# Kernel tuning notes

Measured on AMD Instinct MI355X. Metric: run time of the kernel, lower is better.

The kernel has to match this reference:

```python
import jax, jax.numpy as jnp
import numpy as np

N, SP, SI, K = 256, 64, 32, 8
CIN, C, HEADS, DH = 32, 128, 8, 16
G = 32
OCC_THRESH = 0.7

def _lrelu(x):
    return jax.nn.leaky_relu(x, 0.01)

def _ln(x):
    mu = x.mean(-1, keepdims=True)
    var = ((x - mu) ** 2).mean(-1, keepdims=True)
    return (x - mu) * jax.lax.rsqrt(var + 1e-5)

def _interp3d(vol, coords):
    # vol [C,D,H,W]; coords [...,3] in (z,y,x) voxel-index units -> [..., C]
    v = jnp.moveaxis(vol, 0, -1)
    Dv, Hv, Wv = v.shape[0], v.shape[1], v.shape[2]
    z = jnp.clip(coords[..., 0], 0.0, Dv - 1.0)
    y = jnp.clip(coords[..., 1], 0.0, Hv - 1.0)
    x = jnp.clip(coords[..., 2], 0.0, Wv - 1.0)
    z0 = jnp.floor(z).astype(jnp.int32); y0 = jnp.floor(y).astype(jnp.int32); x0 = jnp.floor(x).astype(jnp.int32)
    z1 = jnp.minimum(z0 + 1, Dv - 1); y1 = jnp.minimum(y0 + 1, Hv - 1); x1 = jnp.minimum(x0 + 1, Wv - 1)
    wz = (z - z0)[..., None]; wy = (y - y0)[..., None]; wx = (x - x0)[..., None]
    c00 = v[z0, y0, x0] * (1 - wx) + v[z0, y0, x1] * wx
    c01 = v[z0, y1, x0] * (1 - wx) + v[z0, y1, x1] * wx
    c10 = v[z1, y0, x0] * (1 - wx) + v[z1, y0, x1] * wx
    c11 = v[z1, y1, x0] * (1 - wx) + v[z1, y1, x1] * wx
    return (c00 * (1 - wy) + c01 * wy) * (1 - wz) + (c10 * (1 - wy) + c11 * wy) * wz

def _tpoints(T, p):
    return p @ T[:3, :3].T + T[:3, 3]

def _rot(T, v):
    return v @ T[:3, :3].T

def _ray_box(o, d, obj_from_cam, dim):
    oo = _tpoints(obj_from_cam, o); dd = _rot(obj_from_cam, d)
    half = dim / 2
    invd = 1.0 / jnp.where(jnp.abs(dd) < 1e-9, 1e-9, dd)
    t0 = (-half - oo) * invd; t1 = (half - oo) * invd
    tlo = jnp.minimum(t0, t1).max(-1); thi = jnp.maximum(t0, t1).min(-1)
    valid = thi >= jnp.maximum(tlo, 0.0)
    return jnp.where(valid, tlo, jnp.inf)

def _attn_block(x, Wqkv, bqkv, Wo, bo, Wf1, bf1, Wf2, bf2):
    # pre-LN MHA over axis -2, then pre-LN FFN; residuals
    h = _ln(x)
    qkv = h @ Wqkv + bqkv
    q, k, v = jnp.split(qkv, 3, axis=-1)
    hd = lambda a: a.reshape(a.shape[:-1] + (HEADS, DH))
    q, k, v = hd(q), hd(k), hd(v)
    s = jnp.einsum('...qhd,...khd->...hqk', q, k) / jnp.sqrt(jnp.float32(DH))
    a = jax.nn.softmax(s, axis=-1)
    o = jnp.einsum('...hqk,...khd->...qhd', a, v)
    o = o.reshape(o.shape[:-2] + (HEADS * DH,)) @ Wo + bo
    x = x + o
    h = _ln(x)
    return x + (_lrelu(h @ Wf1 + bf1) @ Wf2 + bf2)

def setup_inputs() -> dict:
    key = jax.random.key(0)
    ks = jax.random.split(key, 40)
    d = jnp.concatenate([0.25 * (jax.random.uniform(ks[0], (N, 2)) * 2 - 1), jnp.ones((N, 1))], -1)
    rays_d = d / jnp.linalg.norm(d, axis=-1, keepdims=True)
    rays_o = jnp.zeros((N, 3))
    pose = jnp.eye(4).at[2, 3].set(2.0)
    dimension = jnp.ones((3,))
    w = lambda k_, sh: 0.05 * jax.random.normal(k_, sh)
    return {
        'rays_o': rays_o, 'rays_d': rays_d, 'pose': pose, 'dimension': dimension,
        'voxel_probs': jax.random.uniform(ks[1], (G, G, G)),
        'feature_vol': 0.5 * jax.random.normal(ks[2], (CIN, G, G, G)),
        'feature_vol_highres': 0.5 * jax.random.normal(ks[3], (K, 6, G, G, G)),
        'u_primary': jax.random.uniform(ks[4], (N, SP)),
        'u_cat': jax.random.uniform(ks[5], (N, SI)),
        'u_lam': jax.random.uniform(ks[6], (N, SI)),
        'dW1': w(ks[7], (CIN + 1, C)), 'db1': jnp.zeros((C,)),
        'dW2': w(ks[8], (C, 1)), 'db2': jnp.zeros((1,)),
        'rW0': w(ks[9], (CIN + 10, C)), 'rb0': jnp.zeros((C,)),
        'nf_qkv': w(ks[10], (C, 3 * C)), 'nf_qkvb': jnp.zeros((3 * C,)),
        'nf_o': w(ks[11], (C, C)), 'nf_ob': jnp.zeros((C,)),
        'nf_f1': w(ks[12], (C, 2 * C)), 'nf_f1b': jnp.zeros((2 * C,)),
        'nf_f2': w(ks[13], (2 * C, C)), 'nf_f2b': jnp.zeros((C,)),
        'rt_qkv': w(ks[14], (C, 3 * C)), 'rt_qkvb': jnp.zeros((3 * C,)),
        'rt_o': w(ks[15], (C, C)), 'rt_ob': jnp.zeros((C,)),
        'rt_f1': w(ks[16], (C, 2 * C)), 'rt_f1b': jnp.zeros((2 * C,)),
        'rt_f2': w(ks[17], (2 * C, C)), 'rt_f2b': jnp.zeros((C,)),
        'fW': w(ks[18], (C, 3)), 'fb': jnp.zeros((3,)),
        'n_samples_primary': SP, 'n_samples_importance': SI,
    }

def reference(rays_o, rays_d, pose, dimension, voxel_probs, feature_vol, feature_vol_highres,
              u_primary, u_cat, u_lam,
              dW1, db1, dW2, db2, rW0, rb0,
              nf_qkv, nf_qkvb, nf_o, nf_ob, nf_f1, nf_f1b, nf_f2, nf_f2b,
              rt_qkv, rt_qkvb, rt_o, rt_ob, rt_f1, rt_f1b, rt_f2, rt_f2b,
              fW, fb, n_samples_primary, n_samples_importance):
    SPn, SIn = n_samples_primary, n_samples_importance
    ofc = jnp.linalg.inv(pose)  # obj_from_cam
    t_near = _ray_box(rays_o, rays_d, ofc, dimension)
    t_max = t_near + 10.0 * jnp.abs(dimension).sum()
    p_max = rays_o + t_max[:, None] * rays_d
    t_far = t_max - _ray_box(p_max, -rays_d, ofc, dimension)
    m = jnp.isfinite(t_near) & jnp.isfinite(t_far) & (t_far > t_near)
    tn = jnp.where(m, t_near, 0.0); tf = jnp.where(m, t_far, 1.0)
    # stratified primary samples within [t_near, t_far]
    t_coarse = tn[:, None] + (tf - tn)[:, None] * (jnp.arange(SPn, dtype=jnp.float32) + u_primary) / SPn
    get_pts = lambda t: rays_o[:, None] + t[..., None] * rays_d[:, None]
    p_coarse = get_pts(t_coarse)
    def ncoords(p, shp):
        uvz = 0.5 + _tpoints(ofc, p) / dimension
        return uvz[..., ::-1] * (jnp.array(shp, jnp.float32) - 1.0)
    occ_coarse = _interp3d(voxel_probs[None], ncoords(p_coarse, voxel_probs.shape))[..., 0]
    x_coarse = _interp3d(feature_vol, ncoords(p_coarse, feature_vol.shape[-3:]))
    # importance sampling via inverse CDF over adjacent-bin occupancy
    probs = jnp.clip(occ_coarse[:, :-1] + occ_coarse[:, 1:], 1e-12, None)
    cdf = jnp.cumsum(probs, -1)
    cdf = cdf / cdf[:, -1:]
    inds = jnp.clip((u_cat[:, :, None] >= cdf[:, None, :]).sum(-1), 0, SPn - 2)
    t_fine = u_lam * jnp.take_along_axis(t_coarse, inds, -1) + (1 - u_lam) * jnp.take_along_axis(t_coarse, inds + 1, -1)
    p_fine = get_pts(t_fine)
    occ_fine = _interp3d(voxel_probs[None], ncoords(p_fine, voxel_probs.shape))[..., 0]
    x_fine = _interp3d(feature_vol, ncoords(p_fine, feature_vol.shape[-3:]))
    # merge + sort along sample axis
    t_all = jnp.concatenate([t_coarse, t_fine], -1)
    perm = jnp.argsort(t_all, -1)
    t = jnp.take_along_axis(t_all, perm, -1)
    occ = jnp.take_along_axis(jnp.concatenate([occ_coarse, occ_fine], -1), perm, -1)
    p = jnp.take_along_axis(jnp.concatenate([p_coarse, p_fine], -2), perm[..., None], -2)
    x = jnp.take_along_axis(jnp.concatenate([x_coarse, x_fine], -2), perm[..., None], -2)
    # density MLP
    xx = jnp.concatenate([x, occ[..., None]], -1)
    sigma = jax.nn.sigmoid((_lrelu(xx @ dW1 + db1) @ dW2 + db2)[..., 0])
    occ = jnp.where(occ < OCC_THRESH, 0.0, occ)
    alpha = occ * sigma
    # high-res per-view features
    coords_hr = ncoords(p, feature_vol_highres.shape[-3:])
    x_hr = jax.vmap(_interp3d, in_axes=(0, None))(feature_vol_highres, coords_hr)  # [K,N,S,6]
    x_hr = jnp.moveaxis(x_hr, 0, -2)  # [N,S,K,6]
    R = ofc[:3, :3]
    rdo = rays_d @ R.T
    Kv = x_hr.shape[-2]
    bs = x.shape[:2]
    xx2 = jnp.concatenate([
        jnp.broadcast_to(x[:, :, None, :], bs + (Kv, x.shape[-1])),
        x_hr[..., 0:3],
        x_hr[..., 3:6] @ R.T,
        jnp.broadcast_to(rdo[:, None, None, :], bs + (Kv, 3)),
        jnp.broadcast_to(occ[..., None, None], bs + (Kv, 1)),
    ], -1)  # [N,S,K,CIN+10]
    h = xx2 @ rW0 + rb0
    h = _attn_block(h, nf_qkv, nf_qkvb, nf_o, nf_ob, nf_f1, nf_f1b, nf_f2, nf_f2b)  # over views K
    h = h.mean(-2)  # [N,S,C]
    h = _attn_block(h, rt_qkv, rt_qkvb, rt_o, rt_ob, rt_f1, rt_f1b, rt_f2, rt_f2b)  # over samples S
    radiance = jax.nn.sigmoid(h @ fW + fb)  # [N,S,3]
    mk = m[:, None]
    t = jnp.where(mk, t, 0.0)
    occ = jnp.where(mk, occ, 0.0)
    alpha = jnp.where(mk, alpha, 0.0)
    radiance = jnp.where(m[:, None, None], radiance, 0.0)
    # trailing object axis (n_objects=1), matching movedim(0,-1)
    return t[..., None], alpha[..., None], occ[..., None], radiance[..., None]
```

## Files before the change

kernel.cpp:

```cpp
#include <hip/hip_runtime.h>
#include <hip/hip_bf16.h>
#include <cmath>


using bf16 = __hip_bfloat16;
#define DEV __device__ __forceinline__

typedef __attribute__((ext_vector_type(8))) short short8;
typedef __attribute__((ext_vector_type(4))) float f32x4;

DEV float s2f(short s){ unsigned u=((unsigned)(unsigned short)s)<<16; float f; __builtin_memcpy(&f,&u,4); return f; }
DEV short f2s(float f){ bf16 h=__float2bfloat16(f); short r; __builtin_memcpy(&r,&h,2); return r; }

constexpr int NRAY=256, SP=64, SI=32, S=96, KHR=8, CIN=32, C=128, NH=8, DH=16;
constexpr int NT = NRAY*S;
constexpr int MTOT = NT*KHR;

constexpr size_t OFF_RI=0, OFF_TR=9, OFF_M=16, OFF_TN=272, OFF_TF=528, OFF_RDO=784,
  OFF_TS=1552, OFF_OCCS=26128, OFF_OCCT=50704, OFF_CRD=75280, OFF_XS=149008, F32_CNT=935440;

constexpr size_t WT_W0=0, WT_NQKV=8192, WT_NO=57344, WT_NF1=73728, WT_NF2=106496,
  WT_RQKV=139264, WT_RO=188416, WT_RF1=204800, WT_RF2=237568, WT_TOT=270336;
constexpr size_t H2OFF=WT_TOT;
constexpr size_t CHB=H2OFF+(size_t)NT*128;
constexpr size_t RT_TOT=(size_t)NT*512;

struct Corn { int off[8]; float wz, wy, wx; };

DEV void make_corners(float cz, float cy, float cx, Corn& Cn){
  cz=fminf(fmaxf(cz,0.f),31.f); cy=fminf(fmaxf(cy,0.f),31.f); cx=fminf(fmaxf(cx,0.f),31.f);
  int z0=(int)cz, y0=(int)cy, x0=(int)cx;
  int z1=(z0+1<31)?z0+1:31, y1=(y0+1<31)?y0+1:31, x1=(x0+1<31)?x0+1:31;
  Cn.wz=cz-(float)z0; Cn.wy=cy-(float)y0; Cn.wx=cx-(float)x0;
  int zy00=z0*1024+y0*32, zy01=z0*1024+y1*32, zy10=z1*1024+y0*32, zy11=z1*1024+y1*32;
  Cn.off[0]=zy00+x0; Cn.off[1]=zy00+x1;
  Cn.off[2]=zy01+x0; Cn.off[3]=zy01+x1;
  Cn.off[4]=zy10+x0; Cn.off[5]=zy10+x1;
  Cn.off[6]=zy11+x0; Cn.off[7]=zy11+x1;
}

DEV float interp1(const float* __restrict__ vol, const Corn& Cn){
  float v000=vol[Cn.off[0]], v001=vol[Cn.off[1]];
  float v010=vol[Cn.off[2]], v011=vol[Cn.off[3]];
  float v100=vol[Cn.off[4]], v101=vol[Cn.off[5]];
  float v110=vol[Cn.off[6]], v111=vol[Cn.off[7]];
  float wx=Cn.wx, wy=Cn.wy, wz=Cn.wz;
  float c00=v000*(1.f-wx)+v001*wx, c01=v010*(1.f-wx)+v011*wx;
  float c10=v100*(1.f-wx)+v101*wx, c11=v110*(1.f-wx)+v111*wx;
  return (c00*(1.f-wy)+c01*wy)*(1.f-wz) + (c10*(1.f-wy)+c11*wy)*wz;
}

DEV float ray_box(const float* Ri, const float* tr, const float* o3, const float* d3, const float* half){
  float tlo=-INFINITY, thi=INFINITY;
  for(int j=0;j<3;j++){
    float oo=Ri[j*3+0]*o3[0]+Ri[j*3+1]*o3[1]+Ri[j*3+2]*o3[2]+tr[j];
    float dd=Ri[j*3+0]*d3[0]+Ri[j*3+1]*d3[1]+Ri[j*3+2]*d3[2];
    if (fabsf(dd)<1e-9f) dd=1e-9f;
    float inv=1.f/dd;
    float t0=(-half[j]-oo)*inv, t1=(half[j]-oo)*inv;
    tlo=fmaxf(tlo,fminf(t0,t1)); thi=fminf(thi,fmaxf(t0,t1));
  }
  bool valid = thi >= fmaxf(tlo,0.f);
  return valid ? tlo : INFINITY;
}

__global__ __launch_bounds__(64) void k0_setup(
  const float* __restrict__ rays_o, const float* __restrict__ rays_d,
  const float* __restrict__ pose, const float* __restrict__ dimv,
  float* __restrict__ wsf)
{
  __shared__ float Ri[9], tr[3];
  int tid=threadIdx.x; int ray=blockIdx.x*64+tid;
  if(tid==0){
    float P[16];
    for(int j=0;j<16;j++) P[j]=pose[j];
    float a00=P[0],a01=P[1],a02=P[2],a10=P[4],a11=P[5],a12=P[6],a20=P[8],a21=P[9],a22=P[10];
    float c00=a11*a22-a12*a21, c01=a12*a20-a10*a22, c02=a10*a21-a11*a20;
    float det=a00*c00+a01*c01+a02*c02;
    float id=1.f/det;
    Ri[0]=c00*id; Ri[1]=(a02*a21-a01*a22)*id; Ri[2]=(a01*a12-a02*a11)*id;
    Ri[3]=c01*id; Ri[4]=(a00*a22-a02*a20)*id; Ri[5]=(a02*a10-a00*a12)*id;
    Ri[6]=c02*id; Ri[7]=(a01*a20-a00*a21)*id; Ri[8]=(a00*a11-a01*a10)*id;
    float t0=P[3],t1=P[7],t2=P[11];
    tr[0]=-(Ri[0]*t0+Ri[1]*t1+Ri[2]*t2);
    tr[1]=-(Ri[3]*t0+Ri[4]*t1+Ri[5]*t2);
    tr[2]=-(Ri[6]*t0+Ri[7]*t1+Ri[8]*t2);
    if(blockIdx.x==0){
      for(int j=0;j<9;j++) wsf[OFF_RI+j]=Ri[j];
      for(int j=0;j<3;j++) wsf[OFF_TR+j]=tr[j];
    }
  }
  __syncthreads();
  float o3[3],d3[3],dim[3],half[3];
  for(int j=0;j<3;j++){ o3[j]=rays_o[ray*3+j]; d3[j]=rays_d[ray*3+j];
                        dim[j]=dimv[j]; half[j]=0.5f*dim[j]; }
  float tnear=ray_box(Ri,tr,o3,d3,half);
  float tmax=tnear+10.f*(fabsf(dim[0])+fabsf(dim[1])+fabsf(dim[2]));
  float pm[3]={o3[0]+tmax*d3[0], o3[1]+tmax*d3[1], o3[2]+tmax*d3[2]};
  float nd[3]={-d3[0],-d3[1],-d3[2]};
  float tfar=tmax-ray_box(Ri,tr,pm,nd,half);
  bool mm = isfinite(tnear)&&isfinite(tfar)&&(tfar>tnear);
  wsf[OFF_M+ray]=mm?1.f:0.f;
  wsf[OFF_TN+ray]=mm?tnear:0.f;
  wsf[OFF_TF+ray]=mm?tfar:1.f;
  for(int j=0;j<3;j++)
    wsf[OFF_RDO+(size_t)ray*3+j]=Ri[j*3+0]*d3[0]+Ri[j*3+1]*d3[1]+Ri[j*3+2]*d3[2];
}

__global__ __launch_bounds__(128) void k1_sample(
  const float* __restrict__ rays_o, const float* __restrict__ rays_d, const float* __restrict__ dimv,
  const float* __restrict__ voxel, const float* __restrict__ fvol,
  const float* __restrict__ u_p, const float* __restrict__ u_cat, const float* __restrict__ u_lam,
  float* __restrict__ wsf)
{
  int i=blockIdx.x, tid=threadIdx.x;
  __shared__ float Ri[9], tr[3], dim[3], o3[3], d3[3];
  __shared__ float t_all[S], occ_all[S], crd_sh[S][3];
  __shared__ int   coff[S][8];
  __shared__ float cww[S][3];
  __shared__ float cdf[SP];
  __shared__ float totv;
  __shared__ int   rnk[S];
  if(tid<9) Ri[tid]=wsf[OFF_RI+tid];
  if(tid<3){ tr[tid]=wsf[OFF_TR+tid]; dim[tid]=dimv[tid];
             o3[tid]=rays_o[i*3+tid]; d3[tid]=rays_d[i*3+tid]; }
  __syncthreads();
  float tn=wsf[OFF_TN+i], tf=wsf[OFF_TF+i];

  auto do_sample=[&](int s, float t){
    float px=o3[0]+t*d3[0], py=o3[1]+t*d3[1], pz=o3[2]+t*d3[2];
    float q0=Ri[0]*px+Ri[1]*py+Ri[2]*pz+tr[0];
    float q1=Ri[3]*px+Ri[4]*py+Ri[5]*pz+tr[1];
    float q2=Ri[6]*px+Ri[7]*py+Ri[8]*pz+tr[2];
    float cz=(0.5f+q2/dim[2])*31.f;
    float cy=(0.5f+q1/dim[1])*31.f;
    float cx=(0.5f+q0/dim[0])*31.f;
    crd_sh[s][0]=cz; crd_sh[s][1]=cy; crd_sh[s][2]=cx;
    Corn Cn; make_corners(cz,cy,cx,Cn);
    for(int q=0;q<8;q++) coff[s][q]=Cn.off[q];
    cww[s][0]=Cn.wz; cww[s][1]=Cn.wy; cww[s][2]=Cn.wx;
    occ_all[s]=interp1(voxel,Cn);
    t_all[s]=t;
  };

  if(tid<SP){
    float u=u_p[i*SP+tid];
    float t=tn+(tf-tn)*((float)tid+u)*(1.f/64.f);
    do_sample(tid,t);
  }
  __syncthreads();
  if(tid==0){
    float c=0;
    for(int j=0;j<SP-1;j++){ float pr=occ_all[j]+occ_all[j+1]; pr=fmaxf(pr,1e-12f); c+=pr; cdf[j]=c; }
    totv=c;
  }
  __syncthreads();
  if(tid<SP-1) cdf[tid]=cdf[tid]/totv;
  __syncthreads();
  if(tid<SI){
    float u=u_cat[i*SI+tid];
    int cnt=0;
    for(int j=0;j<SP-1;j++) cnt += (u>=cdf[j])?1:0;
    int ind=(cnt<SP-2)?cnt:(SP-2);
    float lam=u_lam[i*SI+tid];
    float tfine=lam*t_all[ind]+(1.f-lam)*t_all[ind+1];
    do_sample(SP+tid,tfine);
  }
  __syncthreads();
  if(tid<S){
    float ts=t_all[tid]; int r=0;
    for(int j=0;j<S;j++){ float tj=t_all[j]; r += (tj<ts || (tj==ts && j<tid)) ? 1:0; }
    rnk[tid]=r;
    size_t base=(size_t)i*S+r;
    wsf[OFF_TS+base]=ts;
    wsf[OFF_OCCS+base]=occ_all[tid];
    wsf[OFF_CRD+base*3+0]=crd_sh[tid][0];
    wsf[OFF_CRD+base*3+1]=crd_sh[tid][1];
    wsf[OFF_CRD+base*3+2]=crd_sh[tid][2];
  }
  __syncthreads();
  for(int idx=tid; idx<S*CIN; idx+=128){
    int s=idx>>5, c=idx&31;
    float wz=cww[s][0], wy=cww[s][1], wx=cww[s][2];
    const float* vc=fvol+(size_t)c*32768;
    float v000=vc[coff[s][0]], v001=vc[coff[s][1]];
    float v010=vc[coff[s][2]], v011=vc[coff[s][3]];
    float v100=vc[coff[s][4]], v101=vc[coff[s][5]];
    float v110=vc[coff[s][6]], v111=vc[coff[s][7]];
    float c00=v000*(1.f-wx)+v001*wx, c01=v010*(1.f-wx)+v011*wx;
    float c10=v100*(1.f-wx)+v101*wx, c11=v110*(1.f-wx)+v111*wx;
    float val=(c00*(1.f-wy)+c01*wy)*(1.f-wz)+(c10*(1.f-wy)+c11*wy)*wz;
    wsf[OFF_XS+((size_t)i*S+rnk[s])*CIN+c]=val;
  }
}

__global__ __launch_bounds__(128) void k2_sigma(
  const float* __restrict__ dW1, const float* __restrict__ db1,
  const float* __restrict__ dW2, const float* __restrict__ db2,
  float* __restrict__ wsf, float* __restrict__ out)
{
  int t=blockIdx.x, tid=threadIdx.x, i=t/S;
  __shared__ float xx[33];
  __shared__ float part[2];
  if(tid<32) xx[tid]=wsf[OFF_XS+(size_t)t*32+tid];
  if(tid==32) xx[32]=wsf[OFF_OCCS+t];
  __syncthreads();
  float acc=db1[tid];
  for(int k=0;k<33;k++) acc=fmaf(xx[k], dW1[k*C+tid], acc);
  acc = acc>=0.f?acc:0.01f*acc;
  float g = acc*dW2[tid];
  for(int off=32;off;off>>=1) g+=__shfl_down(g,off,64);
  if((tid&63)==0) part[tid>>6]=g;
  __syncthreads();
  if(tid==0){
    float z=part[0]+part[1]+db2[0];
    float sg=1.f/(1.f+expf(-z));
    float occ=xx[32];
    float occt=occ<0.7f?0.f:occ;
    float alpha=occt*sg;
    float m=wsf[OFF_M+i];
    float ts=wsf[OFF_TS+t];
    out[t]      =m!=0.f?ts:0.f;
    out[NT+t]   =m!=0.f?alpha:0.f;
    out[2*NT+t] =m!=0.f?occt:0.f;
    wsf[OFF_OCCT+t]=occt;
  }
}

__global__ __launch_bounds__(256) void k_wprep(
  const float* __restrict__ w0, const float* __restrict__ nqkv, const float* __restrict__ no_,
  const float* __restrict__ nf1, const float* __restrict__ nf2,
  const float* __restrict__ rqkv, const float* __restrict__ ro_,
  const float* __restrict__ rf1, const float* __restrict__ rf2,
  short* __restrict__ WT)
{
  int gid = blockIdx.x*256+threadIdx.x;
  if(gid>=(int)WT_TOT) return;
  const float* src; int K,N,Kp; int base;
  if(gid<8192){src=w0;K=42;N=128;Kp=64;base=0;}
  else if(gid<57344){src=nqkv;K=128;N=384;Kp=128;base=8192;}
  else if(gid<73728){src=no_;K=128;N=128;Kp=128;base=57344;}
  else if(gid<106496){src=nf1;K=128;N=256;Kp=128;base=73728;}
  else if(gid<139264){src=nf2;K=256;N=128;Kp=256;base=106496;}
  else if(gid<188416){src=rqkv;K=128;N=384;Kp=128;base=139264;}
  else if(gid<204800){src=ro_;K=128;N=128;Kp=128;base=188416;}
  else if(gid<237568){src=rf1;K=128;N=256;Kp=128;base=204800;}
  else {src=rf2;K=256;N=128;Kp=256;base=237568;}
  int local=gid-base; int n=local/Kp, k=local%Kp;
  WT[gid] = (k<K)? f2s(src[(size_t)k*N+n]) : (short)0;
}

__global__ __launch_bounds__(64) void k_build(
  const float* __restrict__ fvhr, const float* __restrict__ wsf,
  short* __restrict__ X2, int tok0)
{
  int tloc=blockIdx.x, tid=threadIdx.x;
  int t=tok0+tloc, i=t/S;
  __shared__ float hr[KHR][6];
  __shared__ float xf[32];
  __shared__ float RiS[9];
  __shared__ float geo[4];
  __shared__ float crd[3];
  if(tid<9) RiS[tid]=wsf[OFF_RI+tid];
  if(tid>=16&&tid<19) crd[tid-16]=wsf[OFF_CRD+(size_t)t*3+(tid-16)];
  if(tid>=32) xf[tid-32]=wsf[OFF_XS+(size_t)t*32+(tid-32)];
  if(tid==9) geo[0]=wsf[OFF_OCCT+t];
  if(tid>=12&&tid<15) geo[1+(tid-12)]=wsf[OFF_RDO+(size_t)i*3+(tid-12)];
  __syncthreads();
  if(tid<48){
    int k=tid/6, ch=tid%6;
    Corn Cn; make_corners(crd[0],crd[1],crd[2],Cn);
    hr[k][ch]=interp1(fvhr+(size_t)(k*6+ch)*32768, Cn);
  }
  __syncthreads();
  for(int idx=tid; idx<512; idx+=64){
    int k=idx>>6, j=idx&63; float v;
    if(j<32) v=xf[j];
    else if(j<35) v=hr[k][j-32];
    else if(j<38){int r=j-35; v=hr[k][3]*RiS[r*3+0]+hr[k][4]*RiS[r*3+1]+hr[k][5]*RiS[r*3+2];}
    else if(j<41) v=geo[1+(j-38)];
    else if(j==41) v=geo[0];
    else v=0.f;
    X2[(size_t)(tloc*8+k)*64 + j]=f2s(v);
  }
}

template<int K, bool LNA, bool ACT, bool RESID, bool MEAN=false>
__global__ __launch_bounds__(256) void gemm_ln(
  const short* __restrict__ A, const short* __restrict__ Bt,
  const float* __restrict__ bias, const short* __restrict__ Rres,
  short* __restrict__ Cg, int N)
{
  static_assert(!LNA || K==128, "LNA requires K==128");
  constexpr int KSA = (K<128)?K:128;
  constexpr int NSA = K/KSA;
  constexpr int LDA = KSA+8;
  constexpr int LDB = 64+8;
  __shared__ short Al[128*LDA];
  __shared__ short Bl[128*LDB];
  const int tid=threadIdx.x;
  const int bm=blockIdx.x*128, bn=blockIdx.y*128;
  const int lane=tid&63, wave=tid>>6;
  const int wm=(wave>>1)*64, wn=(wave&1)*64;
  const int quad=lane>>4, m16=lane&15;
  f32x4 acc[4][4];
  for(int a=0;a<4;a++) for(int b=0;b<4;b++) acc[a][b]=(f32x4){0.f,0.f,0.f,0.f};

  for(int sa=0; sa<NSA; ++sa){
    if(sa>0) __syncthreads();
    constexpr int CH8=KSA/8;
    for(int it=0; it<(128*CH8)/256; ++it){
      int li=it*256+tid; int row=li/CH8, kc=li%CH8;
      short8 v = *(const short8*)(A + (size_t)(bm+row)*K + sa*KSA + kc*8);
      if constexpr(LNA){
        float f[8]; float ls=0.f,lq=0.f;
        for(int e=0;e<8;e++){ f[e]=s2f(v[e]); ls+=f[e]; lq+=f[e]*f[e]; }
        for(int off=8;off;off>>=1){ ls+=__shfl_xor(ls,off,16); lq+=__shfl_xor(lq,off,16); }
        float mu=ls*(1.f/128.f);
        float var=lq*(1.f/128.f)-mu*mu;
        float rs=rsqrtf(var+1e-5f);
        for(int e=0;e<8;e++) v[e]=f2s((f[e]-mu)*rs);
      }
      *(short8*)&Al[row*LDA+kc*8]=v;
    }
    __syncthreads();
    for(int sb=0; sb<KSA/64; ++sb){
      if(sb>0) __syncthreads();
      for(int it=0; it<4; ++it){
        int li=it*256+tid; int row=li>>3, kc=li&7;
        *(short8*)&Bl[row*LDB+kc*8] =
          *(const short8*)(Bt + (size_t)(bn+row)*K + sa*KSA + sb*64 + kc*8);
      }
      __syncthreads();
      for(int kk=0; kk<64; kk+=32){
        int ka = sb*64+kk;
        short8 af[4], bfv[4];
        for(int im=0; im<4; im++)
          af[im] = *(const short8*)&Al[(wm+im*16+m16)*LDA + ka + quad*8];
        for(int in=0; in<4; in++)
          bfv[in] = *(const short8*)&Bl[(wn+in*16+m16)*LDB + kk + quad*8];
        for(int im=0;im<4;im++)
          for(int in=0;in<4;in++)
            acc[im][in] = __builtin_amdgcn_mfma_f32_16x16x32_bf16(af[im], bfv[in], acc[im][in], 0,0,0);
      }
    }
  }
  for(int in=0;in<4;in++){
    int col = bn + wn + in*16 + m16;
    float bv = bias[col];
    for(int im=0;im<4;im++){
      if constexpr(MEAN){
        float s4=0.f;
        for(int r=0;r<4;r++){
          int grow = bm + wm + im*16 + quad*4 + r;
          float v = acc[im][in][r] + bv;
          if constexpr(RESID) v += s2f(Rres[(size_t)grow*N + col]);
          s4 += v;
        }
        float stok = s4 + __shfl_xor(s4, 16, 64);
        if((quad&1)==0){
          int tok = ((bm + wm + im*16)>>3) + (quad>>1);
          Cg[(size_t)tok*128 + col] = f2s(stok*0.125f);
        }
      } else {
        for(int r=0;r<4;r++){
          int grow = bm + wm + im*16 + quad*4 + r;
          float v = acc[im][in][r] + bv;
          if constexpr(ACT) v = v>=0.f? v : 0.01f*v;
          if constexpr(RESID) v += s2f(Rres[(size_t)grow*N + col]);
          Cg[(size_t)grow*N + col] = f2s(v);
        }
      }
    }
  }
}

__global__ __launch_bounds__(256) void nf_attn(const short* __restrict__ qkv, short* __restrict__ att){
  constexpr int QLD=392;
  __shared__ short Qs[4*8*QLD];
  int t0=blockIdx.x*4, tid=threadIdx.x;
  for(int li=tid; li<1536; li+=256){
    int e=li*8;
    int tok=e/3072, rem=e-tok*3072;
    int j=rem/384, k=rem-j*384;
    *(short8*)&Qs[(tok*8+j)*QLD + k] = *(const short8*)(qkv + (size_t)t0*3072 + e);
  }
  __syncthreads();
  int lt=tid>>6, lane=tid&63;
  int h=lane>>3, q=lane&7;
  const short* base = &Qs[(lt*8)*QLD + h*16];
  float qv[16];
  for(int d=0;d<16;d++) qv[d]=s2f(base[q*QLD+d]);
  float sc[8]; float mx=-INFINITY;
  for(int j=0;j<8;j++){
    float a=0;
    for(int d=0;d<16;d++) a+=qv[d]*s2f(base[j*QLD+128+d]);
    a*=0.25f; sc[j]=a; mx=fmaxf(mx,a);
  }
  float se=0;
  for(int j=0;j<8;j++){ sc[j]=expf(sc[j]-mx); se+=sc[j]; }
  float inv=1.f/se;
  float o[16];
  for(int d=0;d<16;d++) o[d]=0.f;
  for(int j=0;j<8;j++){
    float p=sc[j];
    for(int d=0;d<16;d++) o[d]+=p*s2f(base[j*QLD+256+d]);
  }
  short* ob = att + (size_t)(t0*8 + lt*8 + q)*128 + h*16;
  for(int d=0;d<16;d++) ob[d]=f2s(o[d]*inv);
}

__global__ __launch_bounds__(256) void rt_attn(const short* __restrict__ qkvb, short* __restrict__ attout){
  int b=blockIdx.x; int i=b&255, h0=(b>>8)*4; int tid=threadIdx.x;
  __shared__ float kh[96][64], vh[96][64];
  for(int idx=tid; idx<1536; idx+=256){
    int kv = idx>=768; int l = idx - kv*768;
    int j = l>>3, c = l&7;
    size_t base = ((size_t)(i*96+j))*384 + h0*16 + (kv?256:128) + c*8;
    short8 x = *(const short8*)(qkvb+base);
    float* dst = kv? &vh[j][c*8] : &kh[j][c*8];
    for(int e=0;e<8;e++) dst[e]=s2f(x[e]);
  }
  __syncthreads();
  int jh=tid>>7, t2=tid&127;
  int hh=t2>>5, lq=t2&31, h=h0+hh, r0=lq*3;
  float q[3][16];
  for(int rr=0;rr<3;rr++){
    size_t qb=((size_t)(i*96+r0+rr))*384 + h*16;
    short8 a=*(const short8*)(qkvb+qb), bq=*(const short8*)(qkvb+qb+8);
    for(int e=0;e<8;e++){ q[rr][e]=s2f(a[e]); q[rr][8+e]=s2f(bq[e]); }
  }
  float acc[3][16]; float se[3]={0.f,0.f,0.f};
  for(int rr=0;rr<3;rr++) for(int d=0;d<16;d++) acc[rr][d]=0.f;
  const float* kb=&kh[jh*48][hh*16];
  const float* vb=&vh[jh*48][hh*16];
  for(int j=0;j<48;j++){
    const float* kj = kb + j*64;
    float s0=0.f,s1=0.f,s2=0.f;
    for(int d=0;d<16;d++){ float kv_=kj[d];
      s0=fmaf(q[0][d],kv_,s0); s1=fmaf(q[1][d],kv_,s1); s2=fmaf(q[2][d],kv_,s2); }
    float p0=expf(s0*0.25f), p1=expf(s1*0.25f), p2=expf(s2*0.25f);
    se[0]+=p0; se[1]+=p1; se[2]+=p2;
    const float* vj = vb + j*64;
    for(int d=0;d<16;d++){ float vv=vj[d];
      acc[0][d]=fmaf(p0,vv,acc[0][d]); acc[1][d]=fmaf(p1,vv,acc[1][d]); acc[2][d]=fmaf(p2,vv,acc[2][d]); }
  }
  __syncthreads();
  float* pacc=(float*)kh;
  float* pse =(float*)vh;
  if(jh==1){
    for(int rr=0;rr<3;rr++){
      for(int d=0;d<16;d++) pacc[(t2*3+rr)*16+d]=acc[rr][d];
      pse[t2*3+rr]=se[rr];
    }
  }
  __syncthreads();
  if(jh==0){
    for(int rr=0;rr<3;rr++){
      float sv = se[rr] + pse[t2*3+rr];
      float inv = 1.f/sv;
      short8 o0,o1;
      for(int e=0;e<8;e++){
        float a0=acc[rr][e]   + pacc[(t2*3+rr)*16+e];
        float a1=acc[rr][8+e] + pacc[(t2*3+rr)*16+8+e];
        o0[e]=f2s(a0*inv); o1[e]=f2s(a1*inv);
      }
      size_t ob=((size_t)(i*96+r0+rr))*128 + h*16;
      *(short8*)(attout+ob)=o0;
      *(short8*)(attout+ob+8)=o1;
    }
  }
}

__global__ __launch_bounds__(256) void k_rad(
  const short* __restrict__ h3, const float* __restrict__ fW, const float* __restrict__ fb,
  const float* __restrict__ wsf, float* __restrict__ out)
{
  int t=blockIdx.x*256+threadIdx.x;
  if(t>=NT) return;
  int i=t/S;
  float a0=fb[0], a1=fb[1], a2=fb[2];
  for(int c=0;c<C;c++){
    float hv=s2f(h3[(size_t)t*C+c]);
    a0=fmaf(hv,fW[c*3+0],a0);
    a1=fmaf(hv,fW[c*3+1],a1);
    a2=fmaf(hv,fW[c*3+2],a2);
  }
  float m=wsf[OFF_M+i];
  float r0=1.f/(1.f+expf(-a0)), r1=1.f/(1.f+expf(-a1)), r2=1.f/(1.f+expf(-a2));
  size_t ob=3*(size_t)NT+(size_t)t*3;
  out[ob+0]=m!=0.f?r0:0.f;
  out[ob+1]=m!=0.f?r1:0.f;
  out[ob+2]=m!=0.f?r2:0.f;
}

extern "C" void kernel_launch(void* const* d_in, const int* in_sizes, int n_in,
                              void* d_out, int out_size, void* d_ws, size_t ws_size,
                              hipStream_t stream) {
  (void)in_sizes; (void)n_in; (void)out_size;
  const float* rays_o =(const float*)d_in[0];
  const float* rays_d =(const float*)d_in[1];
  const float* pose   =(const float*)d_in[2];
  const float* dimv   =(const float*)d_in[3];
  const float* voxel  =(const float*)d_in[4];
  const float* fvol   =(const float*)d_in[5];
  const float* fvhr   =(const float*)d_in[6];
  const float* u_p    =(const float*)d_in[7];
  const float* u_cat  =(const float*)d_in[8];
  const float* u_lam  =(const float*)d_in[9];
  const float* dW1    =(const float*)d_in[10];
  const float* db1    =(const float*)d_in[11];
  const float* dW2    =(const float*)d_in[12];
  const float* db2    =(const float*)d_in[13];
  const float* rW0    =(const float*)d_in[14];
  const float* rb0    =(const float*)d_in[15];
  const float* nf_qkv =(const float*)d_in[16];
  const float* nf_qkvb=(const float*)d_in[17];
  const float* nf_o   =(const float*)d_in[18];
  const float* nf_ob  =(const float*)d_in[19];
  const float* nf_f1  =(const float*)d_in[20];
  const float* nf_f1b =(const float*)d_in[21];
  const float* nf_f2  =(const float*)d_in[22];
  const float* nf_f2b =(const float*)d_in[23];
  const float* rt_qkv =(const float*)d_in[24];
  const float* rt_qkvb=(const float*)d_in[25];
  const float* rt_o   =(const float*)d_in[26];
  const float* rt_ob  =(const float*)d_in[27];
  const float* rt_f1  =(const float*)d_in[28];
  const float* rt_f1b =(const float*)d_in[29];
  const float* rt_f2  =(const float*)d_in[30];
  const float* rt_f2b =(const float*)d_in[31];
  const float* fW     =(const float*)d_in[32];
  const float* fb     =(const float*)d_in[33];

  float* wsf=(float*)d_ws;
  short* wsb=(short*)((char*)d_ws + F32_CNT*4);
  float* out=(float*)d_out;

  int nch=8;
  for(int c=1;c<=8;c<<=1){
    size_t mc_=(size_t)MTOT/c;
    size_t region=mc_*640ULL; if(region<RT_TOT) region=RT_TOT;
    size_t need=F32_CNT*4 + 2ULL*(CHB + region);
    if(need <= ws_size){ nch=c; break; }
  }
  const size_t mc = (size_t)MTOT/nch;
  const int Tc = (int)(mc/8);

  short* WT  = wsb;
  short* H2  = wsb + H2OFF;
  short* arena = wsb + CHB;
  short* o_h0 = arena;
  short* o_qkv= arena + (size_t)128*mc;
  short* o_x1 = arena + (size_t)128*mc;
  short* o_f1 = arena + (size_t)256*mc;
  short* o_att= arena + (size_t)512*mc;
  short* o_x2 = arena + (size_t)512*mc;
  short* r_qkv= arena;
  short* r_att= arena + (size_t)384*NT;
  short* r_x  = arena;
  short* r_f1 = arena + (size_t)128*NT;
  short* r_h3 = arena + (size_t)384*NT;

  k0_setup<<<NRAY/64,64,0,stream>>>(rays_o,rays_d,pose,dimv,wsf);
  k1_sample<<<NRAY,128,0,stream>>>(rays_o,rays_d,dimv,voxel,fvol,u_p,u_cat,u_lam,wsf);
  k2_sigma<<<NT,128,0,stream>>>(dW1,db1,dW2,db2,wsf,out);
  k_wprep<<<(int)((WT_TOT+255)/256),256,0,stream>>>(rW0,nf_qkv,nf_o,nf_f1,nf_f2,rt_qkv,rt_o,rt_f1,rt_f2,WT);

  const int mt=(int)(mc/128);
  for(int ch=0; ch<nch; ++ch){
    int tok0 = ch*Tc;
    k_build<<<Tc,64,0,stream>>>(fvhr, wsf, o_x2, tok0);
    gemm_ln< 64,false,false,false><<<dim3(mt,1),256,0,stream>>>(o_x2, WT+WT_W0,  rb0,     nullptr, o_h0, 128);
    gemm_ln<128,true ,false,false><<<dim3(mt,3),256,0,stream>>>(o_h0, WT+WT_NQKV,nf_qkvb, nullptr, o_qkv,384);
    nf_attn<<<Tc/4,256,0,stream>>>(o_qkv, o_att);
    gemm_ln<128,false,false,true ><<<dim3(mt,1),256,0,stream>>>(o_att,WT+WT_NO,  nf_ob,   o_h0,    o_x1, 128);
    gemm_ln<128,true ,true ,false><<<dim3(mt,2),256,0,stream>>>(o_x1, WT+WT_NF1, nf_f1b,  nullptr, o_f1, 256);
    gemm_ln<256,false,false,true ,true><<<dim3(mt,1),256,0,stream>>>(o_f1, WT+WT_NF2, nf_f2b, o_x1,
                                                                     H2+(size_t)tok0*128, 128);
  }

  gemm_ln<128,true ,false,false><<<dim3(NT/128,3),256,0,stream>>>(H2,   WT+WT_RQKV,rt_qkvb, nullptr, r_qkv,384);
  rt_attn<<<NRAY*2,256,0,stream>>>(r_qkv, r_att);
  gemm_ln<128,false,false,true ><<<dim3(NT/128,1),256,0,stream>>>(r_att,WT+WT_RO,  rt_ob,   H2,      r_x,  128);
  gemm_ln<128,true ,true ,false><<<dim3(NT/128,2),256,0,stream>>>(r_x,  WT+WT_RF1, rt_f1b,  nullptr, r_f1, 256);
  gemm_ln<256,false,false,true ><<<dim3(NT/128,1),256,0,stream>>>(r_f1, WT+WT_RF2, rt_f2b,  r_x,     r_h3, 128);
  k_rad<<<NT/256,256,0,stream>>>(r_h3, fW, fb, wsf, out);
}
```

Before: 536.3 us.

## Fuse view-attention QKV GEMM with attention and FFN1 with FFN2 plus mean

Replaces the separate LN+QKV GEMM and neighbour-view attention kernels with one kernel that normalises a 32-row tile, computes QKV with MFMA into shared memory, and runs the 8-view attention in place. Likewise fuses the FFN first GEMM (LN, leaky ReLU) and second GEMM (residual, mean over views) so the 256-wide intermediate stays in shared memory. This removes the large QKV and F1 intermediate round-trips to global memory and two launches per chunk. In exchange the fused kernels use small 32-row tiles and reload the full weight matrices per block, which lowers MFMA reuse and may add shared-memory pressure.

```diff
diff --git a/kernel.cpp b/kernel.cpp
--- a/kernel.cpp
+++ b/kernel.cpp
@@ -285,7 +285,7 @@
   }
 }
 
-template<int K, bool LNA, bool ACT, bool RESID, bool MEAN=false>
+template<int K, bool LNA, bool ACT, bool RESID>
 __global__ __launch_bounds__(256) void gemm_ln(
   const short* __restrict__ A, const short* __restrict__ Bt,
   const float* __restrict__ bias, const short* __restrict__ Rres,
@@ -349,52 +349,75 @@
     int col = bn + wn + in*16 + m16;
     float bv = bias[col];
     for(int im=0;im<4;im++){
-      if constexpr(MEAN){
-        float s4=0.f;
-        for(int r=0;r<4;r++){
-          int grow = bm + wm + im*16 + quad*4 + r;
-          float v = acc[im][in][r] + bv;
-          if constexpr(RESID) v += s2f(Rres[(size_t)grow*N + col]);
-          s4 += v;
-        }
-        float stok = s4 + __shfl_xor(s4, 16, 64);
-        if((quad&1)==0){
-          int tok = ((bm + wm + im*16)>>3) + (quad>>1);
-          Cg[(size_t)tok*128 + col] = f2s(stok*0.125f);
-        }
-      } else {
-        for(int r=0;r<4;r++){
-          int grow = bm + wm + im*16 + quad*4 + r;
-          float v = acc[im][in][r] + bv;
-          if constexpr(ACT) v = v>=0.f? v : 0.01f*v;
-          if constexpr(RESID) v += s2f(Rres[(size_t)grow*N + col]);
-          Cg[(size_t)grow*N + col] = f2s(v);
-        }
+      for(int r=0;r<4;r++){
+        int grow = bm + wm + im*16 + quad*4 + r;
+        float v = acc[im][in][r] + bv;
+        if constexpr(ACT) v = v>=0.f? v : 0.01f*v;
+        if constexpr(RESID) v += s2f(Rres[(size_t)grow*N + col]);
+        Cg[(size_t)grow*N + col] = f2s(v);
       }
     }
   }
 }
 
-__global__ __launch_bounds__(256) void nf_attn(const short* __restrict__ qkv, short* __restrict__ att){
-  constexpr int QLD=392;
-  __shared__ short Qs[4*8*QLD];
-  int t0=blockIdx.x*4, tid=threadIdx.x;
-  for(int li=tid; li<1536; li+=256){
-    int e=li*8;
-    int tok=e/3072, rem=e-tok*3072;
-    int j=rem/384, k=rem-j*384;
-    *(short8*)&Qs[(tok*8+j)*QLD + k] = *(const short8*)(qkv + (size_t)t0*3072 + e);
-  }
-  __syncthreads();
-  int lt=tid>>6, lane=tid&63;
-  int h=lane>>3, q=lane&7;
-  const short* base = &Qs[(lt*8)*QLD + h*16];
+__global__ __launch_bounds__(256) void nf_qkv_attn(
+  const short* __restrict__ A, const short* __restrict__ Bt,
+  const float* __restrict__ bias, short* __restrict__ att)
+{
+  __shared__ short Al[32*136];
+  __shared__ short Bl[384*40];
+  __shared__ short Qt[32*392];
+  const int tid=threadIdx.x;
+  const int bm=blockIdx.x*32;
+  for(int it=0; it<2; ++it){
+    int li=it*256+tid; int row=li>>4, kc=li&15;
+    short8 v = *(const short8*)(A + (size_t)(bm+row)*128 + kc*8);
+    float f[8]; float ls=0.f,lq=0.f;
+    for(int e=0;e<8;e++){ f[e]=s2f(v[e]); ls+=f[e]; lq+=f[e]*f[e]; }
+    for(int off=8;off;off>>=1){ ls+=__shfl_xor(ls,off,16); lq+=__shfl_xor(lq,off,16); }
+    float mu=ls*(1.f/128.f);
+    float var=lq*(1.f/128.f)-mu*mu;
+    float rs=rsqrtf(var+1e-5f);
+    for(int e=0;e<8;e++) v[e]=f2s((f[e]-mu)*rs);
+    *(short8*)&Al[row*136+kc*8]=v;
+  }
+  const int lane=tid&63, wave=tid>>6;
+  const int quad=lane>>4, m16=lane&15;
+  const int wn=wave*96;
+  f32x4 acc[2][6];
+  for(int a=0;a<2;a++) for(int b=0;b<6;b++) acc[a][b]=(f32x4){0.f,0.f,0.f,0.f};
+  for(int kc2=0;kc2<4;++kc2){
+    __syncthreads();
+    for(int it=0; it<6; ++it){
+      int li=it*256+tid; int row=li>>2, c=li&3;
+      *(short8*)&Bl[row*40+c*8] = *(const short8*)(Bt + (size_t)row*128 + kc2*32 + c*8);
+    }
+    __syncthreads();
+    int ka=kc2*32;
+    short8 af[2], bfv[6];
+    af[0]=*(const short8*)&Al[m16*136 + ka + quad*8];
+    af[1]=*(const short8*)&Al[(16+m16)*136 + ka + quad*8];
+    for(int in=0;in<6;in++) bfv[in]=*(const short8*)&Bl[(wn+in*16+m16)*40 + quad*8];
+    for(int im=0;im<2;im++)
+      for(int in=0;in<6;in++)
+        acc[im][in]=__builtin_amdgcn_mfma_f32_16x16x32_bf16(af[im],bfv[in],acc[im][in],0,0,0);
+  }
+  for(int in=0;in<6;in++){
+    int col=wn+in*16+m16;
+    float bv=bias[col];
+    for(int im=0;im<2;im++)
+      for(int r=0;r<4;r++)
+        Qt[(im*16+quad*4+r)*392+col]=f2s(acc[im][in][r]+bv);
+  }
+  __syncthreads();
+  int tok=tid>>6, h=(tid>>3)&7, q=tid&7;
+  const short* base=&Qt[(tok*8)*392 + h*16];
   float qv[16];
-  for(int d=0;d<16;d++) qv[d]=s2f(base[q*QLD+d]);
+  for(int d=0;d<16;d++) qv[d]=s2f(base[q*392+d]);
   float sc[8]; float mx=-INFINITY;
   for(int j=0;j<8;j++){
     float a=0;
-    for(int d=0;d<16;d++) a+=qv[d]*s2f(base[j*QLD+128+d]);
+    for(int d=0;d<16;d++) a+=qv[d]*s2f(base[j*392+128+d]);
     a*=0.25f; sc[j]=a; mx=fmaxf(mx,a);
   }
   float se=0;
@@ -404,10 +427,109 @@
   for(int d=0;d<16;d++) o[d]=0.f;
   for(int j=0;j<8;j++){
     float p=sc[j];
-    for(int d=0;d<16;d++) o[d]+=p*s2f(base[j*QLD+256+d]);
-  }
-  short* ob = att + (size_t)(t0*8 + lt*8 + q)*128 + h*16;
-  for(int d=0;d<16;d++) ob[d]=f2s(o[d]*inv);
+    for(int d=0;d<16;d++) o[d]+=p*s2f(base[j*392+256+d]);
+  }
+  short8 o0,o1;
+  for(int e=0;e<8;e++){ o0[e]=f2s(o[e]*inv); o1[e]=f2s(o[8+e]*inv); }
+  size_t ob=(size_t)(bm+tok*8+q)*128 + h*16;
+  *(short8*)(att+ob)=o0;
+  *(short8*)(att+ob+8)=o1;
+}
+
+__global__ __launch_bounds__(256) void nf_f1f2(
+  const short* __restrict__ X1, const short* __restrict__ Bt1, const float* __restrict__ b1,
+  const short* __restrict__ Bt2, const float* __restrict__ b2,
+  short* __restrict__ H2)
+{
+  __shared__ short Al[32*136];
+  __shared__ short Bl[256*40];
+  __shared__ short F1[32*264];
+  const int tid=threadIdx.x;
+  const int bm=blockIdx.x*32;
+  for(int it=0; it<2; ++it){
+    int li=it*256+tid; int row=li>>4, kc=li&15;
+    short8 v = *(const short8*)(X1 + (size_t)(bm+row)*128 + kc*8);
+    float f[8]; float ls=0.f,lq=0.f;
+    for(int e=0;e<8;e++){ f[e]=s2f(v[e]); ls+=f[e]; lq+=f[e]*f[e]; }
+    for(int off=8;off;off>>=1){ ls+=__shfl_xor(ls,off,16); lq+=__shfl_xor(lq,off,16); }
+    float mu=ls*(1.f/128.f);
+    float var=lq*(1.f/128.f)-mu*mu;
+    float rs=rsqrtf(var+1e-5f);
+    for(int e=0;e<8;e++) v[e]=f2s((f[e]-mu)*rs);
+    *(short8*)&Al[row*136+kc*8]=v;
+  }
+  const int lane=tid&63, wave=tid>>6;
+  const int quad=lane>>4, m16=lane&15;
+  {
+    const int wn=wave*64;
+    f32x4 acc[2][4];
+    for(int a=0;a<2;a++) for(int b=0;b<4;b++) acc[a][b]=(f32x4){0.f,0.f,0.f,0.f};
+    for(int kc2=0;kc2<4;++kc2){
+      __syncthreads();
+      for(int it=0; it<4; ++it){
+        int li=it*256+tid; int row=li>>2, c=li&3;
+        *(short8*)&Bl[row*40+c*8] = *(const short8*)(Bt1 + (size_t)row*128 + kc2*32 + c*8);
+      }
+      __syncthreads();
+      int ka=kc2*32;
+      short8 af[2], bfv[4];
+      af[0]=*(const short8*)&Al[m16*136 + ka + quad*8];
+      af[1]=*(const short8*)&Al[(16+m16)*136 + ka + quad*8];
+      for(int in=0;in<4;in++) bfv[in]=*(const short8*)&Bl[(wn+in*16+m16)*40 + quad*8];
+      for(int im=0;im<2;im++)
+        for(int in=0;in<4;in++)
+          acc[im][in]=__builtin_amdgcn_mfma_f32_16x16x32_bf16(af[im],bfv[in],acc[im][in],0,0,0);
+    }
+    for(int in=0;in<4;in++){
+      int col=wn+in*16+m16;
+      float bv=b1[col];
+      for(int im=0;im<2;im++)
+        for(int r=0;r<4;r++){
+          float v=acc[im][in][r]+bv;
+          v = v>=0.f? v : 0.01f*v;
+          F1[(im*16+quad*4+r)*264+col]=f2s(v);
+        }
+    }
+  }
+  __syncthreads();
+  {
+    const int wn=wave*32;
+    f32x4 acc[2][2];
+    for(int a=0;a<2;a++) for(int b=0;b<2;b++) acc[a][b]=(f32x4){0.f,0.f,0.f,0.f};
+    for(int kc2=0;kc2<8;++kc2){
+      __syncthreads();
+      for(int it=0; it<2; ++it){
+        int li=it*256+tid; int row=li>>2, c=li&3;
+        *(short8*)&Bl[row*40+c*8] = *(const short8*)(Bt2 + (size_t)row*256 + kc2*32 + c*8);
+      }
+      __syncthreads();
+      int ka=kc2*32;
+      short8 af[2], bfv[2];
+      af[0]=*(const short8*)&F1[m16*264 + ka + quad*8];
+      af[1]=*(const short8*)&F1[(16+m16)*264 + ka + quad*8];
+      for(int in=0;in<2;in++) bfv[in]=*(const short8*)&Bl[(wn+in*16+m16)*40 + quad*8];
+      for(int im=0;im<2;im++)
+        for(int in=0;in<2;in++)
+          acc[im][in]=__builtin_amdgcn_mfma_f32_16x16x32_bf16(af[im],bfv[in],acc[im][in],0,0,0);
+    }
+    for(int in=0;in<2;in++){
+      int col=wn+in*16+m16;
+      float bv=b2[col];
+      for(int im=0;im<2;im++){
+        float s4=0.f;
+        for(int r=0;r<4;r++){
+          int grow=bm+im*16+quad*4+r;
+          float v=acc[im][in][r]+bv + s2f(X1[(size_t)grow*128+col]);
+          s4+=v;
+        }
+        float stok = s4 + __shfl_xor(s4,16,64);
+        if((quad&1)==0){
+          int tok=((bm+im*16)>>3)+(quad>>1);
+          H2[(size_t)tok*128+col]=f2s(stok*0.125f);
+        }
+      }
+    }
+  }
 }
 
 __global__ __launch_bounds__(256) void rt_attn(const short* __restrict__ qkvb, short* __restrict__ attout){
@@ -551,9 +673,7 @@
   short* H2  = wsb + H2OFF;
   short* arena = wsb + CHB;
   short* o_h0 = arena;
-  short* o_qkv= arena + (size_t)128*mc;
   short* o_x1 = arena + (size_t)128*mc;
-  short* o_f1 = arena + (size_t)256*mc;
   short* o_att= arena + (size_t)512*mc;
   short* o_x2 = arena + (size_t)512*mc;
   short* r_qkv= arena;
@@ -568,16 +688,15 @@
   k_wprep<<<(int)((WT_TOT+255)/256),256,0,stream>>>(rW0,nf_qkv,nf_o,nf_f1,nf_f2,rt_qkv,rt_o,rt_f1,rt_f2,WT);
 
   const int mt=(int)(mc/128);
+  const int mt32=(int)(mc/32);
   for(int ch=0; ch<nch; ++ch){
     int tok0 = ch*Tc;
     k_build<<<Tc,64,0,stream>>>(fvhr, wsf, o_x2, tok0);
     gemm_ln< 64,false,false,false><<<dim3(mt,1),256,0,stream>>>(o_x2, WT+WT_W0,  rb0,     nullptr, o_h0, 128);
-    gemm_ln<128,true ,false,false><<<dim3(mt,3),256,0,stream>>>(o_h0, WT+WT_NQKV,nf_qkvb, nullptr, o_qkv,384);
-    nf_attn<<<Tc/4,256,0,stream>>>(o_qkv, o_att);
+    nf_qkv_attn<<<mt32,256,0,stream>>>(o_h0, WT+WT_NQKV, nf_qkvb, o_att);
     gemm_ln<128,false,false,true ><<<dim3(mt,1),256,0,stream>>>(o_att,WT+WT_NO,  nf_ob,   o_h0,    o_x1, 128);
-    gemm_ln<128,true ,true ,false><<<dim3(mt,2),256,0,stream>>>(o_x1, WT+WT_NF1, nf_f1b,  nullptr, o_f1, 256);
-    gemm_ln<256,false,false,true ,true><<<dim3(mt,1),256,0,stream>>>(o_f1, WT+WT_NF2, nf_f2b, o_x1,
-                                                                     H2+(size_t)tok0*128, 128);
+    nf_f1f2<<<mt32,256,0,stream>>>(o_x1, WT+WT_NF1, nf_f1b, WT+WT_NF2, nf_f2b,
+                                   H2+(size_t)tok0*128);
   }
 
   gemm_ln<128,true ,false,false><<<dim3(NT/128,3),256,0,stream>>>(H2,   WT+WT_RQKV,rt_qkvb, nullptr, r_qkv,384);
```

New measurement: 514.0 us. -4.2%, faster.
